# Optimization experiments

Measured on AMD Instinct MI355X. Metric: run time of the kernel, lower is better.

Reference implementation:

```python
import jax, jax.numpy as jnp
import numpy as np

B, N, D = 4, 1024, 1024      # batch, seq_len, d_model
H, DK, DV = 16, 64, 64       # n_head, d_k, d_v


def setup_inputs() -> dict:
    key = jax.random.key(0)
    ks = jax.random.split(key, 6)
    xavier = (2.0 / (D + DK)) ** 0.5  # xavier_normal_ std for (d_model, d_k) fan
    return {
        "q": jax.random.normal(ks[0], (B, N, D), jnp.float32),
        "k": jax.random.normal(ks[1], (B, N, D), jnp.float32),
        "v": jax.random.normal(ks[2], (B, N, D), jnp.float32),
        "weight_qs": xavier * jax.random.normal(ks[3], (H, D, DK), jnp.float32),
        "weight_ks": xavier * jax.random.normal(ks[4], (H, D, DK), jnp.float32),
        "weight_vs": xavier * jax.random.normal(ks[5], (H, D, DV), jnp.float32),
    }


def reference(q, k, v, weight_qs, weight_ks, weight_vs):
    # Per-head projections (torch: repeat batch over heads + bmm with (H,D,DK) weights)
    h, d_model, d_k = weight_qs.shape
    scale = 1.0 / (d_k ** 0.5)
    qh = jnp.einsum('bnd,hdk->hbnk', q, weight_qs)   # (H,B,N,DK)
    kh = jnp.einsum('bmd,hdk->hbmk', k, weight_ks)   # (H,B,M,DK)
    vh = jnp.einsum('bmd,hdv->hbmv', v, weight_vs)   # (H,B,M,DV)
    scores = jnp.einsum('hbnk,hbmk->hbnm', qh, kh) * scale  # (H,B,N,M)
    attn = jax.nn.softmax(scores, axis=-1)
    # dropout is identity in eval/deterministic mode
    out = jnp.einsum('hbnm,hbmv->hbnv', attn, vh)    # (H,B,N,DV)
    # torch: split head-stacked batch dim and cat along feature dim -> (B,N,H*DV)
    out = jnp.transpose(out, (1, 2, 0, 3)).reshape(out.shape[1], out.shape[2], -1)
    attn = attn.reshape(h * attn.shape[1], attn.shape[2], attn.shape[3])  # (H*B,N,M)
    return out, attn
```

## Files before the change

kernel.cpp:

```cpp
#include <hip/hip_runtime.h>

typedef short short8 __attribute__((ext_vector_type(8)));
typedef short short4_ __attribute__((ext_vector_type(4)));
typedef float f32x4 __attribute__((ext_vector_type(4)));

#define GLD16(gsrc, ldst) \
  __builtin_amdgcn_global_load_lds((__attribute__((address_space(1))) const void*)(gsrc), \
                                   (__attribute__((address_space(3))) void*)(ldst), 16, 0, 0)

#define BAR() do { asm volatile("s_waitcnt lgkmcnt(0)" ::: "memory"); \
  __builtin_amdgcn_sched_barrier(0); __builtin_amdgcn_s_barrier(); } while (0)

static __device__ __forceinline__ short f2bf(float f) {
  union { float f; unsigned u; } x; x.f = f;
  unsigned r = x.u + 0x7fffu + ((x.u >> 16) & 1u);
  return (short)(r >> 16);
}
static __device__ __forceinline__ float bf2f(unsigned short h) {
  union { unsigned u; float f; } x; x.u = ((unsigned)h) << 16;
  return x.f;
}

__global__ __launch_bounds__(256) void cast_pack(
    const float* __restrict__ q, const float* __restrict__ k, const float* __restrict__ v,
    const float* __restrict__ wq, const float* __restrict__ wk, const float* __restrict__ wv,
    short* __restrict__ xq, short* __restrict__ xk, short* __restrict__ xv,
    short* __restrict__ oq, short* __restrict__ ok, short* __restrict__ ov) {
  int z = blockIdx.z;
  if (blockIdx.x < 4096) {
    const float* s = (z == 0) ? q : (z == 1) ? k : v;
    short* d = (z == 0) ? xq : (z == 1) ? xk : xv;
    int i = (blockIdx.x * 256 + threadIdx.x) * 4;
    float4 f = *(const float4*)(s + i);
    short4_ o;
    o[0] = f2bf(f.x); o[1] = f2bf(f.y); o[2] = f2bf(f.z); o[3] = f2bf(f.w);
    *(short4_*)(d + i) = o;
  } else {
    const float* W = (z == 0) ? wq : (z == 1) ? wk : wv;
    int c = blockIdx.x - 4096;
    short* o = ((z == 0) ? oq : (z == 1) ? ok : ov) + (size_t)c * 1024;
    int h = c >> 6, kk = c & 63;
    const float* src = W + (size_t)h * 65536 + kk;
    #pragma unroll
    for (int it = 0; it < 4; ++it) {
      int d = it * 256 + threadIdx.x;
      o[d] = f2bf(src[(size_t)d * 64]);
    }
  }
}

__global__ __launch_bounds__(256) void proj_gemm(
    const short* __restrict__ xq, const short* __restrict__ xk, const short* __restrict__ xv,
    const short* __restrict__ wq, const short* __restrict__ wk, const short* __restrict__ wv,
    short* __restrict__ pq, short* __restrict__ pk, short* __restrict__ pv) {
  int z = blockIdx.z;
  const short* A  = (z == 0) ? xq : (z == 1) ? xk : xv;
  const short* Bt = (z == 0) ? wq : (z == 1) ? wk : wv;
  short* C        = (z == 0) ? pq : (z == 1) ? pk : pv;
  __shared__ __attribute__((aligned(16))) short As[2][128 * 32];
  __shared__ __attribute__((aligned(16))) short Bs[2][128 * 32];
  int t = threadIdx.x, l = t & 63, w = t >> 6;
  int wr = w >> 1, wc = w & 1;
  int lr = l & 15, lk = l >> 4;
  int bm0 = blockIdx.y * 128, bn0 = blockIdx.x * 128;
  const f32x4 Z = {0.f, 0.f, 0.f, 0.f};
  f32x4 acc[4][4];
  #pragma unroll
  for (int m = 0; m < 4; ++m)
    #pragma unroll
    for (int n = 0; n < 4; ++n) acc[m][n] = Z;

  int boff0 = w * 2 * 1024 + l * 16;
  int row0 = boff0 >> 6, ke0 = (boff0 & 63) >> 1;
  int boff1 = boff0 + 1024;
  int row1 = boff1 >> 6, ke1 = (boff1 & 63) >> 1;
  const short* ga0 = A + (size_t)(bm0 + row0) * 1024 + ke0;
  const short* ga1 = A + (size_t)(bm0 + row1) * 1024 + ke1;
  const short* gb0 = Bt + (size_t)(bn0 + row0) * 1024 + ke0;
  const short* gb1 = Bt + (size_t)(bn0 + row1) * 1024 + ke1;
  int lo = (w * 2) * 512, lo1 = (w * 2 + 1) * 512;

  for (int kb = 0; kb < 1024; kb += 64) {
    #pragma unroll
    for (int hh = 0; hh < 2; ++hh) {
      int kc = kb + hh * 32;
      GLD16(ga0 + kc, As[hh] + lo);
      GLD16(ga1 + kc, As[hh] + lo1);
      GLD16(gb0 + kc, Bs[hh] + lo);
      GLD16(gb1 + kc, Bs[hh] + lo1);
    }
    __syncthreads();
    #pragma unroll
    for (int hh = 0; hh < 2; ++hh) {
      short8 a[4], bfr[4];
      #pragma unroll
      for (int m = 0; m < 4; ++m)
        a[m] = *(const short8*)(As[hh] + (wr * 64 + m * 16 + lr) * 32 + lk * 8);
      #pragma unroll
      for (int n = 0; n < 4; ++n)
        bfr[n] = *(const short8*)(Bs[hh] + (wc * 64 + n * 16 + lr) * 32 + lk * 8);
      __builtin_amdgcn_s_setprio(1);
      #pragma unroll
      for (int m = 0; m < 4; ++m)
        #pragma unroll
        for (int n = 0; n < 4; ++n)
          acc[m][n] = __builtin_amdgcn_mfma_f32_16x16x32_bf16(a[m], bfr[n], acc[m][n], 0, 0, 0);
      __builtin_amdgcn_s_setprio(0);
    }
    __syncthreads();
  }
  #pragma unroll
  for (int m = 0; m < 4; ++m)
    #pragma unroll
    for (int n = 0; n < 4; ++n)
      #pragma unroll
      for (int i = 0; i < 4; ++i) {
        int r = bm0 + wr * 64 + m * 16 + lk * 4 + i;
        int cc = bn0 + wc * 64 + n * 16 + lr;
        C[(size_t)r * 1024 + cc] = f2bf(acc[m][n][i]);
      }
}

__global__ __launch_bounds__(256) void vtrans(
    const short* __restrict__ pv, short* __restrict__ vt) {
  __shared__ short T[64 * 72];
  int t = threadIdx.x;
  int hb = blockIdx.y, h = hb >> 2, b = hb & 3;
  int n0 = blockIdx.x * 64;
  const short* src = pv + (size_t)b * 1048576 + (size_t)n0 * 1024 + h * 64;
  #pragma unroll
  for (int it = 0; it < 2; ++it) {
    int id = it * 256 + t;
    int row = id >> 3, seg = id & 7;
    *(short8*)(T + row * 72 + seg * 8) = *(const short8*)(src + (size_t)row * 1024 + seg * 8);
  }
  __syncthreads();
  short* dst = vt + (size_t)hb * 65536 + n0;
  #pragma unroll
  for (int it = 0; it < 2; ++it) {
    int id = it * 256 + t;
    int dv = id >> 3, seg = id & 7;
    short8 vv;
    #pragma unroll
    for (int jj = 0; jj < 8; ++jj) vv[jj] = T[(seg * 8 + jj) * 72 + dv];
    *(short8*)(dst + (size_t)dv * 1024 + seg * 8) = vv;
  }
}

#define PW 72
__global__ __launch_bounds__(512) void attn_fused(
    const short* __restrict__ pq, const short* __restrict__ pk, const short* __restrict__ vt,
    float* __restrict__ dout) {
  __shared__ __attribute__((aligned(16))) short Ks[2][64 * PW];
  __shared__ __attribute__((aligned(16))) short Vs[2][64 * PW];
  __shared__ __attribute__((aligned(16))) short Ps[128 * PW];
  int t = threadIdx.x, l = t & 63, w = t >> 6;
  int lr = l & 15, lk = l >> 4;
  int bid = blockIdx.x;
  int swz = (bid & 7) * 64 + (bid >> 3);
  int hb = swz >> 3, qt = swz & 7;
  int h = hb >> 2, b = hb & 3;
  int q0 = qt * 128;
  const short* Qg = pq + (size_t)b * 1048576 + h * 64;
  const short* Kg = pk + (size_t)b * 1048576 + h * 64;
  const short* Vt = vt + (size_t)hb * 65536;
  float* attnp = dout + 4194304 + (size_t)hb * 1048576;
  const f32x4 Z = {0.f, 0.f, 0.f, 0.f};
  const float scale = 0.125f;
  int r0 = w * 16;
  int sj = t >> 3, sco = (t & 7) * 8;

  const short* qrow = Qg + (size_t)(q0 + r0 + lr) * 1024;
  short8 aq[2];
  aq[0] = *(const short8*)(qrow + lk * 8);
  aq[1] = *(const short8*)(qrow + 32 + lk * 8);

  short8 ka, va;
  ka = *(const short8*)(Kg + (size_t)sj * 1024 + sco);
  *(short8*)(Ks[0] + sj * PW + sco) = ka;
  BAR();

  float s[4] = {0.f, 0.f, 0.f, 0.f};

  for (int nc = 0; nc < 16; ++nc) {
    int cur = nc & 1;
    if (nc < 15)
      ka = *(const short8*)(Kg + (size_t)((nc + 1) * 64 + sj) * 1024 + sco);
    f32x4 acc[4] = {Z, Z, Z, Z};
    __builtin_amdgcn_s_setprio(1);
    #pragma unroll
    for (int kk = 0; kk < 2; ++kk)
      #pragma unroll
      for (int n = 0; n < 4; ++n) {
        short8 bk = *(const short8*)(Ks[cur] + (n * 16 + lr) * PW + kk * 32 + lk * 8);
        acc[n] = __builtin_amdgcn_mfma_f32_16x16x32_bf16(aq[kk], bk, acc[n], 0, 0, 0);
      }
    __builtin_amdgcn_s_setprio(0);
    #pragma unroll
    for (int i = 0; i < 4; ++i)
      s[i] += __expf(acc[0][i] * scale) + __expf(acc[1][i] * scale) +
              __expf(acc[2][i] * scale) + __expf(acc[3][i] * scale);
    if (nc < 15)
      *(short8*)(Ks[cur ^ 1] + sj * PW + sco) = ka;
    BAR();
  }
  #pragma unroll
  for (int i = 0; i < 4; ++i)
    #pragma unroll
    for (int msk = 1; msk < 16; msk <<= 1)
      s[i] += __shfl_xor(s[i], msk, 64);
  float inv[4];
  #pragma unroll
  for (int i = 0; i < 4; ++i) inv[i] = 1.0f / s[i];

  ka = *(const short8*)(Kg + (size_t)sj * 1024 + sco);
  va = *(const short8*)(Vt + (size_t)sj * 1024 + sco);
  *(short8*)(Ks[0] + sj * PW + sco) = ka;
  *(short8*)(Vs[0] + sj * PW + sco) = va;
  BAR();

  f32x4 acco[4] = {Z, Z, Z, Z};
  int prow = r0 + (l >> 2), pseg = (l & 3) * 16;
  float* gpb = attnp + (size_t)(q0 + prow) * 1024 + pseg;
  for (int nc = 0; nc < 16; ++nc) {
    int cur = nc & 1;
    if (nc < 15) {
      ka = *(const short8*)(Kg + (size_t)((nc + 1) * 64 + sj) * 1024 + sco);
      va = *(const short8*)(Vt + (size_t)sj * 1024 + (nc + 1) * 64 + sco);
    }
    f32x4 acc[4] = {Z, Z, Z, Z};
    __builtin_amdgcn_s_setprio(1);
    #pragma unroll
    for (int kk = 0; kk < 2; ++kk)
      #pragma unroll
      for (int n = 0; n < 4; ++n) {
        short8 bk = *(const short8*)(Ks[cur] + (n * 16 + lr) * PW + kk * 32 + lk * 8);
        acc[n] = __builtin_amdgcn_mfma_f32_16x16x32_bf16(aq[kk], bk, acc[n], 0, 0, 0);
      }
    __builtin_amdgcn_s_setprio(0);
    #pragma unroll
    for (int n = 0; n < 4; ++n)
      #pragma unroll
      for (int i = 0; i < 4; ++i) {
        float p = __expf(acc[n][i] * scale) * inv[i];
        Ps[(r0 + lk * 4 + i) * PW + n * 16 + lr] = f2bf(p);
      }
    #pragma unroll
    for (int kk = 0; kk < 2; ++kk) {
      short8 ap = *(const short8*)(Ps + (r0 + lr) * PW + kk * 32 + lk * 8);
      __builtin_amdgcn_s_setprio(1);
      #pragma unroll
      for (int f = 0; f < 4; ++f) {
        short8 bv = *(const short8*)(Vs[cur] + (f * 16 + lr) * PW + kk * 32 + lk * 8);
        acco[f] = __builtin_amdgcn_mfma_f32_16x16x32_bf16(ap, bv, acco[f], 0, 0, 0);
      }
      __builtin_amdgcn_s_setprio(0);
    }
    {
      short8 p0 = *(const short8*)(Ps + prow * PW + pseg);
      short8 p1 = *(const short8*)(Ps + prow * PW + pseg + 8);
      float* gp = gpb + nc * 64;
      float4 f0 = {bf2f((unsigned short)p0[0]), bf2f((unsigned short)p0[1]),
                   bf2f((unsigned short)p0[2]), bf2f((unsigned short)p0[3])};
      float4 f1 = {bf2f((unsigned short)p0[4]), bf2f((unsigned short)p0[5]),
                   bf2f((unsigned short)p0[6]), bf2f((unsigned short)p0[7])};
      float4 f2 = {bf2f((unsigned short)p1[0]), bf2f((unsigned short)p1[1]),
                   bf2f((unsigned short)p1[2]), bf2f((unsigned short)p1[3])};
      float4 f3 = {bf2f((unsigned short)p1[4]), bf2f((unsigned short)p1[5]),
                   bf2f((unsigned short)p1[6]), bf2f((unsigned short)p1[7])};
      *(float4*)gp = f0; *(float4*)(gp + 4) = f1;
      *(float4*)(gp + 8) = f2; *(float4*)(gp + 12) = f3;
    }
    if (nc < 15) {
      *(short8*)(Ks[cur ^ 1] + sj * PW + sco) = ka;
      *(short8*)(Vs[cur ^ 1] + sj * PW + sco) = va;
    }
    BAR();
  }
  #pragma unroll
  for (int f = 0; f < 4; ++f)
    #pragma unroll
    for (int i = 0; i < 4; ++i) {
      int row = q0 + r0 + lk * 4 + i;
      int dv = f * 16 + lr;
      dout[(size_t)b * 1048576 + (size_t)row * 1024 + h * 64 + dv] = acco[f][i];
    }
}

extern "C" void kernel_launch(void* const* d_in, const int* in_sizes, int n_in,
                              void* d_out, int out_size, void* d_ws, size_t ws_size,
                              hipStream_t stream) {
  const void* big[3] = {0, 0, 0};
  const void* small[3] = {0, 0, 0};
  int nb = 0, ns = 0;
  for (int i = 0; i < n_in && i < 6; ++i) {
    if (in_sizes[i] == 4194304) { if (nb < 3) big[nb++] = d_in[i]; }
    else                        { if (ns < 3) small[ns++] = d_in[i]; }
  }
  const float *q, *k, *v, *wq, *wk, *wv;
  if (nb == 3 && ns == 3) {
    q = (const float*)big[0]; k = (const float*)big[1]; v = (const float*)big[2];
    wq = (const float*)small[0]; wk = (const float*)small[1]; wv = (const float*)small[2];
  } else {
    q = (const float*)d_in[0]; k = (const float*)d_in[1]; v = (const float*)d_in[2];
    wq = (const float*)d_in[3]; wk = (const float*)d_in[4]; wv = (const float*)d_in[5];
  }
  short* W   = (short*)d_ws;
  short* xq  = W;
  short* xk  = W + 4194304;
  short* xv  = W + 8388608;
  short* wtq = W + 12582912;
  short* wtk = W + 13631488;
  short* wtv = W + 14680064;
  short* pq  = W + 15728640;
  short* pk  = W + 19922944;
  short* pv  = W + 24117248;
  short* vt  = W + 28311552;
  float* out = (float*)d_out;

  cast_pack<<<dim3(5120, 1, 3), 256, 0, stream>>>(q, k, v, wq, wk, wv,
                                                  xq, xk, xv, wtq, wtk, wtv);
  proj_gemm<<<dim3(8, 32, 3), 256, 0, stream>>>(xq, xk, xv, wtq, wtk, wtv, pq, pk, pv);
  vtrans<<<dim3(16, 64), 256, 0, stream>>>(pv, vt);
  attn_fused<<<dim3(512), 512, 0, stream>>>(pq, pk, vt, out);
}
```

Measured before the change: 189.7 us.

## Swap MFMA operands, XOR-swizzle LDS tiles, and store attention probabilities from registers

```diff
diff --git a/kernel.cpp b/kernel.cpp
--- a/kernel.cpp
+++ b/kernel.cpp
@@ -147,15 +147,15 @@
   }
 }
 
-#define PW 72
 __global__ __launch_bounds__(512) void attn_fused(
     const short* __restrict__ pq, const short* __restrict__ pk, const short* __restrict__ vt,
     float* __restrict__ dout) {
-  __shared__ __attribute__((aligned(16))) short Ks[2][64 * PW];
-  __shared__ __attribute__((aligned(16))) short Vs[2][64 * PW];
-  __shared__ __attribute__((aligned(16))) short Ps[128 * PW];
+  __shared__ __attribute__((aligned(16))) short Ks[2][64 * 64];
+  __shared__ __attribute__((aligned(16))) short Vs[2][64 * 64];
+  __shared__ __attribute__((aligned(16))) short Ps[128 * 64];
   int t = threadIdx.x, l = t & 63, w = t >> 6;
   int lr = l & 15, lk = l >> 4;
+  int r7 = lr & 7;
   int bid = blockIdx.x;
   int swz = (bid & 7) * 64 + (bid >> 3);
   int hb = swz >> 3, qt = swz & 7;
@@ -168,7 +168,8 @@
   const f32x4 Z = {0.f, 0.f, 0.f, 0.f};
   const float scale = 0.125f;
   int r0 = w * 16;
-  int sj = t >> 3, sco = (t & 7) * 8;
+  int sj = t >> 3, slt = t & 7;
+  int stoff = sj * 64 + ((slt ^ (sj & 7)) << 3);
 
   const short* qrow = Qg + (size_t)(q0 + r0 + lr) * 1024;
   short8 aq[2];
@@ -176,57 +177,53 @@
   aq[1] = *(const short8*)(qrow + 32 + lk * 8);
 
   short8 ka, va;
-  ka = *(const short8*)(Kg + (size_t)sj * 1024 + sco);
-  *(short8*)(Ks[0] + sj * PW + sco) = ka;
+  ka = *(const short8*)(Kg + (size_t)sj * 1024 + slt * 8);
+  *(short8*)(Ks[0] + stoff) = ka;
   BAR();
 
-  float s[4] = {0.f, 0.f, 0.f, 0.f};
+  float s = 0.0f;
 
   for (int nc = 0; nc < 16; ++nc) {
     int cur = nc & 1;
     if (nc < 15)
-      ka = *(const short8*)(Kg + (size_t)((nc + 1) * 64 + sj) * 1024 + sco);
+      ka = *(const short8*)(Kg + (size_t)((nc + 1) * 64 + sj) * 1024 + slt * 8);
     f32x4 acc[4] = {Z, Z, Z, Z};
     __builtin_amdgcn_s_setprio(1);
     #pragma unroll
     for (int kk = 0; kk < 2; ++kk)
       #pragma unroll
       for (int n = 0; n < 4; ++n) {
-        short8 bk = *(const short8*)(Ks[cur] + (n * 16 + lr) * PW + kk * 32 + lk * 8);
-        acc[n] = __builtin_amdgcn_mfma_f32_16x16x32_bf16(aq[kk], bk, acc[n], 0, 0, 0);
+        short8 bk = *(const short8*)(Ks[cur] + (n * 16 + lr) * 64 + (((kk * 4 + lk) ^ r7) << 3));
+        acc[n] = __builtin_amdgcn_mfma_f32_16x16x32_bf16(bk, aq[kk], acc[n], 0, 0, 0);
       }
     __builtin_amdgcn_s_setprio(0);
     #pragma unroll
-    for (int i = 0; i < 4; ++i)
-      s[i] += __expf(acc[0][i] * scale) + __expf(acc[1][i] * scale) +
-              __expf(acc[2][i] * scale) + __expf(acc[3][i] * scale);
+    for (int n = 0; n < 4; ++n)
+      s += __expf(acc[n][0] * scale) + __expf(acc[n][1] * scale) +
+           __expf(acc[n][2] * scale) + __expf(acc[n][3] * scale);
     if (nc < 15)
-      *(short8*)(Ks[cur ^ 1] + sj * PW + sco) = ka;
+      *(short8*)(Ks[cur ^ 1] + stoff) = ka;
     BAR();
   }
-  #pragma unroll
-  for (int i = 0; i < 4; ++i)
-    #pragma unroll
-    for (int msk = 1; msk < 16; msk <<= 1)
-      s[i] += __shfl_xor(s[i], msk, 64);
-  float inv[4];
-  #pragma unroll
-  for (int i = 0; i < 4; ++i) inv[i] = 1.0f / s[i];
-
-  ka = *(const short8*)(Kg + (size_t)sj * 1024 + sco);
-  va = *(const short8*)(Vt + (size_t)sj * 1024 + sco);
-  *(short8*)(Ks[0] + sj * PW + sco) = ka;
-  *(short8*)(Vs[0] + sj * PW + sco) = va;
+  s += __shfl_xor(s, 16, 64);
+  s += __shfl_xor(s, 32, 64);
+  float inv = 1.0f / s;
+
+  ka = *(const short8*)(Kg + (size_t)sj * 1024 + slt * 8);
+  va = *(const short8*)(Vt + (size_t)sj * 1024 + slt * 8);
+  *(short8*)(Ks[0] + stoff) = ka;
+  *(short8*)(Vs[0] + stoff) = va;
   BAR();
 
   f32x4 acco[4] = {Z, Z, Z, Z};
-  int prow = r0 + (l >> 2), pseg = (l & 3) * 16;
-  float* gpb = attnp + (size_t)(q0 + prow) * 1024 + pseg;
+  float* arow = attnp + (size_t)(q0 + r0 + lr) * 1024 + lk * 4;
+  short* psrow = Ps + (r0 + lr) * 64;
+  int wsw = (lr & 7) << 1;
   for (int nc = 0; nc < 16; ++nc) {
     int cur = nc & 1;
     if (nc < 15) {
-      ka = *(const short8*)(Kg + (size_t)((nc + 1) * 64 + sj) * 1024 + sco);
-      va = *(const short8*)(Vt + (size_t)sj * 1024 + (nc + 1) * 64 + sco);
+      ka = *(const short8*)(Kg + (size_t)((nc + 1) * 64 + sj) * 1024 + slt * 8);
+      va = *(const short8*)(Vt + (size_t)sj * 1024 + (nc + 1) * 64 + slt * 8);
     }
     f32x4 acc[4] = {Z, Z, Z, Z};
     __builtin_amdgcn_s_setprio(1);
@@ -234,46 +231,36 @@
     for (int kk = 0; kk < 2; ++kk)
       #pragma unroll
       for (int n = 0; n < 4; ++n) {
-        short8 bk = *(const short8*)(Ks[cur] + (n * 16 + lr) * PW + kk * 32 + lk * 8);
-        acc[n] = __builtin_amdgcn_mfma_f32_16x16x32_bf16(aq[kk], bk, acc[n], 0, 0, 0);
+        short8 bk = *(const short8*)(Ks[cur] + (n * 16 + lr) * 64 + (((kk * 4 + lk) ^ r7) << 3));
+        acc[n] = __builtin_amdgcn_mfma_f32_16x16x32_bf16(bk, aq[kk], acc[n], 0, 0, 0);
       }
     __builtin_amdgcn_s_setprio(0);
     #pragma unroll
-    for (int n = 0; n < 4; ++n)
-      #pragma unroll
-      for (int i = 0; i < 4; ++i) {
-        float p = __expf(acc[n][i] * scale) * inv[i];
-        Ps[(r0 + lk * 4 + i) * PW + n * 16 + lr] = f2bf(p);
-      }
+    for (int n = 0; n < 4; ++n) {
+      float e0 = __expf(acc[n][0] * scale) * inv;
+      float e1 = __expf(acc[n][1] * scale) * inv;
+      float e2 = __expf(acc[n][2] * scale) * inv;
+      float e3 = __expf(acc[n][3] * scale) * inv;
+      float4 fo = {e0, e1, e2, e3};
+      *(float4*)(arow + nc * 64 + n * 16) = fo;
+      short4_ p4;
+      p4[0] = f2bf(e0); p4[1] = f2bf(e1); p4[2] = f2bf(e2); p4[3] = f2bf(e3);
+      *(short4_*)(psrow + (((n * 4 + lk) ^ wsw) << 2)) = p4;
+    }
     #pragma unroll
     for (int kk = 0; kk < 2; ++kk) {
-      short8 ap = *(const short8*)(Ps + (r0 + lr) * PW + kk * 32 + lk * 8);
+      short8 ap = *(const short8*)(psrow + (((kk * 4 + lk) ^ r7) << 3));
       __builtin_amdgcn_s_setprio(1);
       #pragma unroll
       for (int f = 0; f < 4; ++f) {
-        short8 bv = *(const short8*)(Vs[cur] + (f * 16 + lr) * PW + kk * 32 + lk * 8);
+        short8 bv = *(const short8*)(Vs[cur] + (f * 16 + lr) * 64 + (((kk * 4 + lk) ^ r7) << 3));
         acco[f] = __builtin_amdgcn_mfma_f32_16x16x32_bf16(ap, bv, acco[f], 0, 0, 0);
       }
       __builtin_amdgcn_s_setprio(0);
     }
-    {
-      short8 p0 = *(const short8*)(Ps + prow * PW + pseg);
-      short8 p1 = *(const short8*)(Ps + prow * PW + pseg + 8);
-      float* gp = gpb + nc * 64;
-      float4 f0 = {bf2f((unsigned short)p0[0]), bf2f((unsigned short)p0[1]),
-                   bf2f((unsigned short)p0[2]), bf2f((unsigned short)p0[3])};
-      float4 f1 = {bf2f((unsigned short)p0[4]), bf2f((unsigned short)p0[5]),
-                   bf2f((unsigned short)p0[6]), bf2f((unsigned short)p0[7])};
-      float4 f2 = {bf2f((unsigned short)p1[0]), bf2f((unsigned short)p1[1]),
-                   bf2f((unsigned short)p1[2]), bf2f((unsigned short)p1[3])};
-      float4 f3 = {bf2f((unsigned short)p1[4]), bf2f((unsigned short)p1[5]),
-                   bf2f((unsigned short)p1[6]), bf2f((unsigned short)p1[7])};
-      *(float4*)gp = f0; *(float4*)(gp + 4) = f1;
-      *(float4*)(gp + 8) = f2; *(float4*)(gp + 12) = f3;
-    }
     if (nc < 15) {
-      *(short8*)(Ks[cur ^ 1] + sj * PW + sco) = ka;
-      *(short8*)(Vs[cur ^ 1] + sj * PW + sco) = va;
+      *(short8*)(Ks[cur ^ 1] + stoff) = ka;
+      *(short8*)(Vs[cur ^ 1] + stoff) = va;
     }
     BAR();
   }
```

Result: faster. 156.9 us, median of 2 (-17.3%).
